# Performance work log

Measured on AMD Instinct MI355X. Metric: run time of the kernel, lower is better.

The kernel has to match this reference:

```python
import jax, jax.numpy as jnp
from jax import lax
import numpy as np

MAX_ITER = 5          # init: max_iter
KSIZE = 3             # init: kernel_size
WEIGHT = 1.0          # init: weight_components
K_COMP = 64           # max number of tracked components (bars) per (b, c)


def setup_inputs() -> dict:
    key = jax.random.key(0)
    k1, k2 = jax.random.split(key)
    predictions = jax.random.normal(k1, (4, 4, 512, 512), dtype=jnp.float32)
    targets = jax.random.randint(k2, (4, 512, 512), 0, 4, dtype=jnp.int32)
    return {"predictions": predictions, "targets": targets}


def _box_sum(x):
    # all-ones KSIZE x KSIZE depthwise conv with SAME zero padding == windowed sum
    return lax.reduce_window(x, 0.0, lax.add, (1, 1, KSIZE, KSIZE), (1, 1, 1, 1), 'SAME')


def _erode(x):
    return (_box_sum(x) == float(KSIZE * KSIZE)).astype(x.dtype)


def _dilate(x):
    return (_box_sum(x) > 0).astype(x.dtype)


def _label_components(fg):
    # fg: bool [B, C, H, W]. 4-connected CCL via min-label propagation to fixpoint;
    # each component gets label = min linear index of its pixels, background = H*W.
    B, C, H, W = fg.shape
    sentinel = jnp.int32(H * W)
    idx = jnp.arange(H * W, dtype=jnp.int32).reshape(1, 1, H, W)
    init = jnp.where(fg, idx, sentinel)

    def nmin(l):
        up = jnp.pad(l, ((0, 0), (0, 0), (1, 0), (0, 0)), constant_values=H * W)[:, :, :-1, :]
        dn = jnp.pad(l, ((0, 0), (0, 0), (0, 1), (0, 0)), constant_values=H * W)[:, :, 1:, :]
        lf = jnp.pad(l, ((0, 0), (0, 0), (0, 0), (1, 0)), constant_values=H * W)[:, :, :, :-1]
        rt = jnp.pad(l, ((0, 0), (0, 0), (0, 0), (0, 1)), constant_values=H * W)[:, :, :, 1:]
        return jnp.minimum(jnp.minimum(up, dn), jnp.minimum(lf, rt))

    def cond(carry):
        return carry[1]

    def body(carry):
        l, _ = carry
        new = jnp.where(fg, jnp.minimum(l, nmin(l)), sentinel)
        return new, jnp.any(new != l)

    labels, _ = lax.while_loop(cond, body, (init, jnp.array(True)))
    return labels


def _component_sizes(im):
    # im: float 0/1 [B, C, H, W] -> top-K_COMP component sizes (sorted desc) [B, C, K_COMP]
    B, C, H, W = im.shape
    HW = H * W
    fg = im > 0.5
    labels = _label_components(fg)
    lab = labels.reshape(B * C, HW)
    w = fg.astype(jnp.float32).reshape(B * C, HW)
    seg = jax.vmap(lambda l, ww: jax.ops.segment_sum(ww, l, num_segments=HW + 1))(lab, w)
    sizes = seg[:, :HW]                      # drop background bucket (label == HW)
    top = lax.top_k(sizes, K_COMP)[0]        # sorted component sizes (barcode at this filtration step)
    return top.reshape(B, C, K_COMP)


def _barcodes(bm):
    # bm: [B, C, H, W] binary maps. Build erosion/dilation filtration exactly as the
    # torch module: image at index max_iter//2 is the original, indices above are
    # successive erosions, indices below are successive dilations.
    mid = MAX_ITER // 2
    imgs = [None] * MAX_ITER
    imgs[mid] = bm
    cur = bm
    for t in range(mid):
        cur = _erode(cur)
        imgs[mid + t + 1] = cur
    cur = bm
    for t in range(mid):
        cur = _dilate(cur)
        imgs[mid - t - 1] = cur
    return jnp.stack([_component_sizes(im) for im in imgs], axis=0)  # [T, B, C, K]


def reference(predictions, targets):
    B, C, H, W = predictions.shape
    prob = jax.nn.softmax(predictions, axis=1)
    pred_cls = jnp.argmax(prob, axis=1)                       # [B, H, W]
    cls = jnp.arange(C, dtype=pred_cls.dtype).reshape(1, -1, 1, 1)
    bp = (pred_cls[:, None] == cls).astype(jnp.float32)       # [B, C, H, W]
    bt = (targets[:, None] == cls).astype(jnp.float32)
    bar_p = _barcodes(bp)                                     # [T, B, C, K]
    bar_t = _barcodes(bt)
    # barcode (persistence-diagram) L1 distance, components matched by size rank,
    # weighted by weight_components; reduction='none' -> per-sample loss [B]
    losses = WEIGHT * jnp.sum(jnp.abs(bar_p - bar_t), axis=(0, 2, 3))
    return losses
```

## Files before the change

kernel.cpp:

```cpp
#include <hip/hip_runtime.h>
#include <stdint.h>

typedef unsigned long long u64;

#define BB   4
#define CC   4
#define HHH  512
#define WWW  512
#define HW   (HHH*WWW)
#define NIMG (BB*CC)
#define NSRC 2
#define NLVL 5
#define NB   (NLVL*NIMG)
#define KTOP 64
#define NBIN 4096
#define WPI  4096
#define SLICE ((size_t)NSRC*NIMG*WPI)
#define TROWS 32
#define TPX  (TROWS*WWW)
#define TWORDS (TROWS*8)
#define NTILE 16
#define NSEAM (NTILE-1)
#define RCAP 8192
#define NGTAG (1 << 30)


__device__ __forceinline__ void unite(int* L, int a, int b) {
  bool done = false;
  do {
    { int p = L[a]; while (p != a) { int gp = L[p]; L[a] = gp; a = gp; p = L[a]; } }
    { int p = L[b]; while (p != b) { int gp = L[p]; L[b] = gp; b = gp; p = L[b]; } }
    if (a < b) {
      int old = atomicMin(&L[b], a);
      done = (old == b);
      b = old;
    } else if (b < a) {
      int old = atomicMin(&L[a], b);
      done = (old == a);
      a = old;
    } else {
      done = true;
    }
  } while (!done);
}

__device__ __forceinline__ int runstart_bit(u64 w, int k) {
  u64 lowz = ~w & ((k == 0) ? 0ull : ((1ull << k) - 1));
  return lowz ? (64 - __clzll(lowz)) : 0;
}

__device__ __forceinline__ u64 morph_word(u64 c0, u64 cm, u64 cp, u64 u0, u64 um, u64 up_,
                                          u64 d0, u64 dm, u64 dp, int erode) {
  u64 v, vm, vp;
  if (erode) {
    v = u0 & c0 & d0; vm = um & cm & dm; vp = up_ & cp & dp;
    return v & ((v << 1) | (vm >> 63)) & ((v >> 1) | (vp << 63));
  } else {
    v = u0 | c0 | d0; vm = um | cm | dm; vp = up_ | cp | dp;
    return v | (v << 1) | (vm >> 63) | (v >> 1) | (vp << 63);
  }
}


__global__ void k_base_mask_bits(const float* __restrict__ pred, const int* __restrict__ tgt,
                                 u64* __restrict__ bm) {
  int i = blockIdx.x * blockDim.x + threadIdx.x;
  if (i >= BB * HW) return;
  int b  = i >> 18;
  int hw = i & (HW - 1);
  float p0 = pred[(b * CC + 0) * HW + hw];
  float p1 = pred[(b * CC + 1) * HW + hw];
  float p2 = pred[(b * CC + 2) * HW + hw];
  float p3 = pred[(b * CC + 3) * HW + hw];
  int amax = 0; float best = p0;
  if (p1 > best) { best = p1; amax = 1; }
  if (p2 > best) { best = p2; amax = 2; }
  if (p3 > best) { best = p3; amax = 3; }
  int tg = tgt[i];
  int lane = threadIdx.x & 63;
  u64* bp = bm + (size_t)(2 * NSRC + 0) * NIMG * WPI;
  u64* bt = bm + (size_t)(2 * NSRC + 1) * NIMG * WPI;
#pragma unroll
  for (int c = 0; c < CC; ++c) {
    u64 wp = __ballot(amax == c);
    u64 wt = __ballot(tg == c);
    if (lane == 0) {
      int wi = ((b * CC + c) << 12) + (hw >> 6);
      bp[wi] = wp;
      bt[wi] = wt;
    }
  }
}

__global__ void k_morph2(u64* __restrict__ bm) {
  __shared__ u64 a[68 * 8];
  __shared__ u64 bsh[66 * 8];
  int blk = blockIdx.x;
  int erode = (blk < 256);
  int blk2 = blk & 255;
  int band = blk2 & 7;
  int imgi = blk2 >> 3;
  int r0 = band * 64;
  const u64* ip = bm + 2 * SLICE + ((size_t)imgi << 12);
  u64* o1 = bm + (erode ? 3 : 1) * SLICE + ((size_t)imgi << 12);
  u64* o2 = bm + (erode ? 4 : 0) * SLICE + ((size_t)imgi << 12);
  int t = threadIdx.x;
  for (int k = t; k < 68 * 8; k += 256) {
    int rr = r0 - 2 + (k >> 3);
    a[k] = (rr >= 0 && rr < HHH) ? ip[rr * 8 + (k & 7)] : 0;
  }
  __syncthreads();
  for (int k = t; k < 66 * 8; k += 256) {
    int j = k >> 3, wc = k & 7;
    int rr = r0 - 1 + j;
    if (rr < 0 || rr >= HHH) { bsh[k] = 0; continue; }
    int ai = (j + 1) * 8 + wc;
    bsh[k] = morph_word(a[ai], wc ? a[ai - 1] : 0, (wc < 7) ? a[ai + 1] : 0,
                        a[ai - 8], wc ? a[ai - 9] : 0, (wc < 7) ? a[ai - 7] : 0,
                        a[ai + 8], wc ? a[ai + 7] : 0, (wc < 7) ? a[ai + 9] : 0, erode);
  }
  __syncthreads();
  for (int k = t; k < 512; k += 256) {
    int j = k >> 3, wc = k & 7;
    int bi = (j + 1) * 8 + wc;
    o1[(r0 + j) * 8 + wc] = bsh[bi];
    o2[(r0 + j) * 8 + wc] =
        morph_word(bsh[bi], wc ? bsh[bi - 1] : 0, (wc < 7) ? bsh[bi + 1] : 0,
                   bsh[bi - 8], wc ? bsh[bi - 9] : 0, (wc < 7) ? bsh[bi - 7] : 0,
                   bsh[bi + 8], wc ? bsh[bi + 7] : 0, (wc < 7) ? bsh[bi + 9] : 0, erode);
  }
}


__global__ __launch_bounds__(1024) void k_ccl_tile(const u64* __restrict__ bm, int src,
                                                   int* __restrict__ labels,
                                                   int* __restrict__ counts,
                                                   int* __restrict__ rootbuf,
                                                   int* __restrict__ rootcnt) {
  __shared__ int par[TPX];
  __shared__ u64 w[TWORDS];
  __shared__ int anyfg, rc;
  int t = threadIdx.x;
  int tile = blockIdx.x;
  int lvl = tile >> 8;
  int img = (tile >> 4) & 15;
  int tin = tile & 15;
  int bimg = tile >> 4;
  int trow0 = tin * TROWS;
  const u64* ib = bm + ((size_t)((lvl * NSRC + src) * NIMG + img) << 12);
  if (t == 0) { anyfg = 0; rc = 0; }
  __syncthreads();
  if (t < TWORDS) {
    u64 wd = ib[trow0 * 8 + t];
    w[t] = wd;
    if (wd) {
      anyfg = 1;
      int segbase = ((t >> 3) << 9) + ((t & 7) << 6);
      u64 hm = wd & ~(wd << 1);
      while (hm) {
        int k = __ffsll(hm) - 1; hm &= hm - 1;
        par[segbase + k] = segbase + k;
      }
    }
  }
  __syncthreads();
  if (!anyfg) { if (t == 0) rootcnt[tile] = 0; return; }
  int wave = t >> 6, lane = t & 63;
  for (int i = wave; i < TWORDS; i += 16) {
    u64 r0 = w[i];
    if (!r0) continue;
    int row = i >> 3, wc = i & 7;
    int segbase = (row << 9) + (wc << 6);
    u64 prev = wc ? w[i - 1] : 0;
    if (lane == 0 && (r0 & 1) && (prev >> 63))
      unite(par, segbase, segbase - 64 + runstart_bit(prev, 63));
    if (row) {
      u64 up = w[i - 8];
      if (up) {
        u64 upprev = wc ? w[i - 9] : 0;
        u64 lsr0 = (r0 << 1) | (prev >> 63);
        u64 lsup = (up << 1) | (upprev >> 63);
        u64 need = r0 & up & ~(lsr0 & lsup);
        if ((need >> lane) & 1)
          unite(par, segbase + runstart_bit(r0, lane),
                     segbase - 512 + runstart_bit(up, lane));
      }
    }
  }
  __syncthreads();
  int off = trow0 * WWW;
  int* L = labels + (bimg << 18) + off;
  for (int i = wave; i < TWORDS; i += 16) {
    u64 wd = w[i];
    if (!wd) continue;
    u64 hm = wd & ~(wd << 1);
    if ((hm >> lane) & 1) {
      int p = ((i >> 3) << 9) + ((i & 7) << 6) + lane;
      int r = p;
      int q = par[r] & 16383;
      while (q != r) { r = q; q = par[r] & 16383; }
      u64 inv = ~(wd >> lane);
      int len = inv ? (__ffsll(inv) - 1) : (64 - lane);
      atomicAdd(&par[r], len << 14);
      int row = i >> 3;
      if (r == p) {
        int idx = atomicAdd(&rc, 1);
        rootbuf[tile * RCAP + idx] = off + p;
        L[p] = off + p;
      } else if (row == 0 || row == TROWS - 1) {
        L[p] = off + r;
      }
    }
  }
  __syncthreads();
  int rcv = rc;
  int base = bimg << 18;
  for (int e = t; e < rcv; e += 1024) {
    int p = rootbuf[tile * RCAP + e] - off;
    counts[base + off + p] = par[p] >> 14;
  }
  if (t == 0) rootcnt[tile] = rcv;
}


__global__ void k_seam_merge(const u64* __restrict__ bm, int src, int* __restrict__ labels) {
  int gid = blockIdx.x * blockDim.x + threadIdx.x;
  int sw = gid >> 6;
  if (sw >= NLVL * NIMG * NSEAM * 8) return;
  int lane = threadIdx.x & 63;
  int lvl = sw / (NIMG * NSEAM * 8);
  int rem = sw - lvl * (NIMG * NSEAM * 8);
  int img = rem / (NSEAM * 8);
  int rem2 = rem - img * (NSEAM * 8);
  int seam = rem2 >> 3, wc = rem2 & 7;
  int rowb = (seam + 1) * TROWS;
  const u64* ib = bm + ((size_t)((lvl * NSRC + src) * NIMG + img) << 12);
  int wb = rowb * 8 + wc;
  u64 r0 = ib[wb];
  if (!r0) return;
  u64 up = ib[wb - 8];
  if (!up) return;
  u64 prev = wc ? ib[wb - 1] : 0;
  u64 upprev = wc ? ib[wb - 9] : 0;
  u64 lsr0 = (r0 << 1) | (prev >> 63);
  u64 lsup = (up << 1) | (upprev >> 63);
  u64 need = r0 & up & ~(lsr0 & lsup);
  if ((need >> lane) & 1) {
    int* L = labels + ((lvl * NIMG + img) << 18);
    int segbase = (rowb << 9) + (wc << 6);
    unite(L, segbase + runstart_bit(r0, lane), segbase - 512 + runstart_bit(up, lane));
  }
}


__global__ __launch_bounds__(256) void k_fixup(const int* __restrict__ rootcnt,
                                               int* __restrict__ rootbuf,
                                               const int* __restrict__ labels,
                                               int* __restrict__ counts,
                                               int* __restrict__ hist,
                                               int* __restrict__ lcount) {
  int tile = blockIdx.x;
  int bimg = tile >> 4;
  int tin = tile & 15;
  int t = threadIdx.x;
  hist[bimg * NBIN + tin * 256 + t] = 0;
  if (t == 0 && tin == 0) lcount[bimg] = 0;
  int n = rootcnt[tile];
  const int* L = labels + (bimg << 18);
  int* cnt = counts + (bimg << 18);
  for (int e = t; e < n; e += 256) {
    int r = rootbuf[tile * RCAP + e];
    int g = r;
    int q = L[g];
    while (q != g) { g = q; q = L[g]; }
    if (g != r) {
      atomicAdd(&cnt[g], cnt[r]);
      rootbuf[tile * RCAP + e] = r | NGTAG;
    }
  }
}


__global__ __launch_bounds__(256) void k_tile_hist(const int* __restrict__ rootcnt,
                                                   const int* __restrict__ rootbuf,
                                                   const int* __restrict__ counts,
                                                   int* __restrict__ hist,
                                                   int* __restrict__ lcount,
                                                   int* __restrict__ lsizes) {
  __shared__ int lh[NBIN];
  int t = threadIdx.x;
  for (int k = t; k < NBIN; k += 256) lh[k] = 0;
  __syncthreads();
  int tile = blockIdx.x;
  int bimg = tile >> 4;
  int n = rootcnt[tile];
  const int* cnt = counts + (bimg << 18);
  for (int e = t; e < n; e += 256) {
    int r = rootbuf[tile * RCAP + e];
    if (r & NGTAG) continue;
    int s = cnt[r];
    if (s <= NBIN) atomicAdd(&lh[s - 1], 1);
    else {
      int idx = atomicAdd(&lcount[bimg], 1);
      if (idx < KTOP) lsizes[bimg * KTOP + idx] = s;
    }
  }
  __syncthreads();
  int* gh = hist + bimg * NBIN;
  for (int k = t; k < NBIN; k += 256)
    if (lh[k]) atomicAdd(&gh[k], lh[k]);
}


__global__ __launch_bounds__(1024) void k_top64(const int* __restrict__ hist,
                                                const int* __restrict__ lcount,
                                                const int* __restrict__ lsizes,
                                                float* __restrict__ top, int src) {
  __shared__ int lh[NBIN];
  __shared__ int sc[1024];
  __shared__ int ls[KTOP];
  int bimg = blockIdx.x;
  int t = threadIdx.x;
  const int* gh = hist + bimg * NBIN;
  for (int k = t; k < NBIN; k += 1024) lh[k] = gh[k];
  int n = lcount[bimg];
  if (n > KTOP) n = KTOP;
  if (t < KTOP) ls[t] = (t < n) ? lsizes[bimg * KTOP + t] : 0;
  int lvl = bimg >> 4, im = bimg & 15;
  float* tp = top + ((size_t)(src * NLVL + lvl) * NIMG + im) * KTOP;
  if (t < KTOP) tp[t] = 0.f;
  __syncthreads();
  if (t < n) {
    int myv = ls[t], rank = 0;
    for (int j = 0; j < n; ++j) {
      int vj = ls[j];
      rank += (vj > myv) || (vj == myv && j < t);
    }
    tp[rank] = (float)myv;
  }
  int base = NBIN - 4 * (t + 1);
  int c = lh[base] + lh[base + 1] + lh[base + 2] + lh[base + 3];
  sc[t] = c;
  __syncthreads();
  for (int off = 1; off < 1024; off <<= 1) {
    int v = (t >= off) ? sc[t - off] : 0;
    __syncthreads();
    sc[t] += v;
    __syncthreads();
  }
  int pos = n + sc[t] - c;
  if (pos < KTOP && c > 0) {
    for (int k = 3; k >= 0 && pos < KTOP; --k) {
      int s = base + k + 1;
      int hc = lh[base + k];
      while (hc-- > 0 && pos < KTOP) tp[pos++] = (float)s;
    }
  }
}

__global__ void k_loss(const float* __restrict__ top, float* __restrict__ out) {
  int b = blockIdx.x;
  int t = threadIdx.x;
  float acc = 0.f;
  const int TOT = NLVL * CC * KTOP;
  for (int e = t; e < TOT; e += 256) {
    int k = e & (KTOP - 1);
    int rest = e >> 6;
    int c = rest & (CC - 1);
    int lvl = rest >> 2;
    int img = b * CC + c;
    size_t iP = ((size_t)(0 * NLVL + lvl) * NIMG + img) * KTOP + k;
    size_t iT = ((size_t)(1 * NLVL + lvl) * NIMG + img) * KTOP + k;
    acc += fabsf(top[iP] - top[iT]);
  }
  __shared__ float r[256];
  r[t] = acc;
  __syncthreads();
  for (int off = 128; off > 0; off >>= 1) {
    if (t < off) r[t] += r[t + off];
    __syncthreads();
  }
  if (t == 0) out[b] = r[0];
}


extern "C" void kernel_launch(void* const* d_in, const int* in_sizes, int n_in,
                              void* d_out, int out_size, void* d_ws, size_t ws_size,
                              hipStream_t stream) {
  const float* pred = (const float*)d_in[0];
  const int*   tgt  = (const int*)d_in[1];
  float* out = (float*)d_out;

  uint8_t* ws = (uint8_t*)d_ws;
  size_t off = 0;
  u64* bmAll   = (u64*)(ws + off); off += (size_t)NLVL * NSRC * NIMG * WPI * 8;
  int* labels  = (int*)(ws + off); off += (size_t)NB * HW * 4;
  int* counts  = (int*)(ws + off); off += (size_t)NB * HW * 4;
  int* rootbuf = (int*)(ws + off); off += (size_t)NB * NTILE * RCAP * 4;
  int* rootcnt = (int*)(ws + off); off += (size_t)NB * NTILE * 4;
  int* hist    = (int*)(ws + off); off += (size_t)NB * NBIN * 4;
  int* lcount  = (int*)(ws + off); off += (size_t)NB * 4;
  int* lsizes  = (int*)(ws + off); off += (size_t)NB * KTOP * 4;
  float* top   = (float*)(ws + off); off += (size_t)NSRC * NLVL * NIMG * KTOP * 4;

  k_base_mask_bits<<<(BB * HW) / 256, 256, 0, stream>>>(pred, tgt, bmAll);
  k_morph2<<<512, 256, 0, stream>>>(bmAll);

  for (int src = 0; src < NSRC; ++src) {
    k_ccl_tile  <<<NB * NTILE, 1024, 0, stream>>>(bmAll, src, labels, counts, rootbuf, rootcnt);
    k_seam_merge<<<(NLVL * NIMG * NSEAM * 8 * 64) / 256, 256, 0, stream>>>(bmAll, src, labels);
    k_fixup     <<<NB * NTILE, 256, 0, stream>>>(rootcnt, rootbuf, labels, counts, hist, lcount);
    k_tile_hist <<<NB * NTILE, 256, 0, stream>>>(rootcnt, rootbuf, counts, hist, lcount, lsizes);
    k_top64     <<<NB, 1024, 0, stream>>>(hist, lcount, lsizes, top, src);
  }

  k_loss<<<BB, 256, 0, stream>>>(top, out);
}
```

Baseline: 195.3 us.

## Use compact per-tile root IDs for global union-find and merge both sources per launch

Tile CCL roots now get compact slot IDs through a shared-memory bitmap plus a prefix-sum, replacing pixel-indexed labels and counts arrays. Global union-find runs over a small per-image root array, and tile boundary rows record root slots so seam merging can look them up. Both sources (prediction and target) are processed in single launches instead of a host loop, which halves the launch count and gives each launch more blocks. Tile blocks are ordered so the middle level is scheduled first. The cost is extra prefix-scan and sync work inside the tile kernel.

```diff
diff --git a/kernel.cpp b/kernel.cpp
--- a/kernel.cpp
+++ b/kernel.cpp
@@ -2,6 +2,7 @@
 #include <stdint.h>
 
 typedef unsigned long long u64;
+typedef unsigned int u32;
 
 #define BB   4
 #define CC   4
@@ -12,6 +13,7 @@
 #define NSRC 2
 #define NLVL 5
 #define NB   (NLVL*NIMG)
+#define NSIMG (NSRC*NB)
 #define KTOP 64
 #define NBIN 4096
 #define WPI  4096
@@ -22,7 +24,7 @@
 #define NTILE 16
 #define NSEAM (NTILE-1)
 #define RCAP 8192
-#define NGTAG (1 << 30)
+#define GSP  (NTILE*RCAP)
 
 
 __device__ __forceinline__ void unite(int* L, int a, int b) {
@@ -47,6 +49,10 @@
 __device__ __forceinline__ int runstart_bit(u64 w, int k) {
   u64 lowz = ~w & ((k == 0) ? 0ull : ((1ull << k) - 1));
   return lowz ? (64 - __clzll(lowz)) : 0;
+}
+
+__device__ __forceinline__ int lvl_of_slot(int s) {
+  return s == 0 ? 2 : s == 1 ? 0 : s == 2 ? 1 : s == 3 ? 3 : 4;
 }
 
 __device__ __forceinline__ u64 morph_word(u64 c0, u64 cm, u64 cp, u64 u0, u64 um, u64 up_,
@@ -78,8 +84,8 @@
   if (p3 > best) { best = p3; amax = 3; }
   int tg = tgt[i];
   int lane = threadIdx.x & 63;
-  u64* bp = bm + (size_t)(2 * NSRC + 0) * NIMG * WPI;
-  u64* bt = bm + (size_t)(2 * NSRC + 1) * NIMG * WPI;
+  u64* bp = bm + 2 * SLICE;
+  u64* bt = bm + 2 * SLICE + (size_t)NIMG * WPI;
 #pragma unroll
   for (int c = 0; c < CC; ++c) {
     u64 wp = __ballot(amax == c);
@@ -132,30 +138,36 @@
 }
 
 
-__global__ __launch_bounds__(1024) void k_ccl_tile(const u64* __restrict__ bm, int src,
-                                                   int* __restrict__ labels,
-                                                   int* __restrict__ counts,
-                                                   int* __restrict__ rootbuf,
+__global__ __launch_bounds__(1024) void k_ccl_tile(const u64* __restrict__ bm,
+                                                   int* __restrict__ bound,
+                                                   int* __restrict__ gparent,
+                                                   int* __restrict__ sizes,
                                                    int* __restrict__ rootcnt) {
   __shared__ int par[TPX];
   __shared__ u64 w[TWORDS];
-  __shared__ int anyfg, rc;
-  int t = threadIdx.x;
-  int tile = blockIdx.x;
-  int lvl = tile >> 8;
-  int img = (tile >> 4) & 15;
-  int tin = tile & 15;
-  int bimg = tile >> 4;
+  __shared__ u32 rb32[TWORDS * 2];
+  __shared__ int rcnt[256];
+  __shared__ int anyfg;
+  int t = threadIdx.x;
+  int idx = blockIdx.x;
+  int lvl = lvl_of_slot(idx >> 9);
+  int rem = idx & 511;
+  int src = rem >> 8;
+  int img = (rem >> 4) & 15;
+  int tin = rem & 15;
+  int simg = src * NB + lvl * NIMG + img;
+  int tile = simg * NTILE + tin;
   int trow0 = tin * TROWS;
   const u64* ib = bm + ((size_t)((lvl * NSRC + src) * NIMG + img) << 12);
-  if (t == 0) { anyfg = 0; rc = 0; }
+  if (t == 0) anyfg = 0;
+  if (t < 512) rb32[t] = 0;
   __syncthreads();
   if (t < TWORDS) {
     u64 wd = ib[trow0 * 8 + t];
     w[t] = wd;
     if (wd) {
       anyfg = 1;
-      int segbase = ((t >> 3) << 9) + ((t & 7) << 6);
+      int segbase = t << 6;
       u64 hm = wd & ~(wd << 1);
       while (hm) {
         int k = __ffsll(hm) - 1; hm &= hm - 1;
@@ -170,7 +182,7 @@
     u64 r0 = w[i];
     if (!r0) continue;
     int row = i >> 3, wc = i & 7;
-    int segbase = (row << 9) + (wc << 6);
+    int segbase = i << 6;
     u64 prev = wc ? w[i - 1] : 0;
     if (lane == 0 && (r0 & 1) && (prev >> 63))
       unite(par, segbase, segbase - 64 + runstart_bit(prev, 63));
@@ -188,51 +200,78 @@
     }
   }
   __syncthreads();
-  int off = trow0 * WWW;
-  int* L = labels + (bimg << 18) + off;
   for (int i = wave; i < TWORDS; i += 16) {
     u64 wd = w[i];
     if (!wd) continue;
     u64 hm = wd & ~(wd << 1);
     if ((hm >> lane) & 1) {
-      int p = ((i >> 3) << 9) + ((i & 7) << 6) + lane;
+      int p = (i << 6) + lane;
       int r = p;
       int q = par[r] & 16383;
       while (q != r) { r = q; q = par[r] & 16383; }
       u64 inv = ~(wd >> lane);
       int len = inv ? (__ffsll(inv) - 1) : (64 - lane);
       atomicAdd(&par[r], len << 14);
-      int row = i >> 3;
-      if (r == p) {
-        int idx = atomicAdd(&rc, 1);
-        rootbuf[tile * RCAP + idx] = off + p;
-        L[p] = off + p;
-      } else if (row == 0 || row == TROWS - 1) {
-        L[p] = off + r;
+      if (r == p) atomicOr(&rb32[p >> 5], 1u << (p & 31));
+    }
+  }
+  __syncthreads();
+  if (t < 256) rcnt[t] = __popcll(((u64)rb32[2 * t + 1] << 32) | rb32[2 * t]);
+  __syncthreads();
+  for (int off2 = 1; off2 < 256; off2 <<= 1) {
+    int v = 0;
+    if (t < 256 && t >= off2) v = rcnt[t - off2];
+    __syncthreads();
+    if (t < 256) rcnt[t] += v;
+    __syncthreads();
+  }
+  if (wave < 16) {
+    int ii = wave;
+    int i = (ii < 8) ? ii : (240 + ii);
+    u64 wd = w[i];
+    if (wd) {
+      u64 hm = wd & ~(wd << 1);
+      if ((hm >> lane) & 1) {
+        int p = (i << 6) + lane;
+        int r = p;
+        int q = par[r] & 16383;
+        while (q != r) { r = q; q = par[r] & 16383; }
+        int wi = r >> 6;
+        u64 rbw = ((u64)rb32[2 * wi + 1] << 32) | rb32[2 * wi];
+        int slot = rcnt[wi] - __popcll(rbw) +
+                   __popcll(rbw & (((u64)1 << (r & 63)) - 1));
+        bound[(size_t)tile * 1024 + (ii < 8 ? 0 : 512) + ((i & 7) << 6) + lane] =
+            tin * RCAP + slot;
       }
     }
   }
-  __syncthreads();
-  int rcv = rc;
-  int base = bimg << 18;
-  for (int e = t; e < rcv; e += 1024) {
-    int p = rootbuf[tile * RCAP + e] - off;
-    counts[base + off + p] = par[p] >> 14;
-  }
-  if (t == 0) rootcnt[tile] = rcv;
-}
-
-
-__global__ void k_seam_merge(const u64* __restrict__ bm, int src, int* __restrict__ labels) {
-  int gid = blockIdx.x * blockDim.x + threadIdx.x;
-  int sw = gid >> 6;
-  if (sw >= NLVL * NIMG * NSEAM * 8) return;
+  int gbase = simg * GSP;
+  for (int i = wave; i < TWORDS; i += 16) {
+    u64 rbw = ((u64)rb32[2 * i + 1] << 32) | rb32[2 * i];
+    if (!((rbw >> lane) & 1)) continue;
+    int p = (i << 6) + lane;
+    int slot = rcnt[i] - __popcll(rbw) + __popcll(rbw & (((u64)1 << lane) - 1));
+    int gid = tin * RCAP + slot;
+    sizes[gbase + gid] = par[p] >> 14;
+    gparent[gbase + gid] = gid;
+  }
+  if (t == 0) rootcnt[tile] = rcnt[255];
+}
+
+
+__global__ void k_seam_merge(const u64* __restrict__ bm, const int* __restrict__ bound,
+                             int* __restrict__ gparent) {
+  int gid_t = blockIdx.x * blockDim.x + threadIdx.x;
+  int sw = gid_t >> 6;
+  if (sw >= NSRC * NLVL * NIMG * NSEAM * 8) return;
   int lane = threadIdx.x & 63;
-  int lvl = sw / (NIMG * NSEAM * 8);
-  int rem = sw - lvl * (NIMG * NSEAM * 8);
-  int img = rem / (NSEAM * 8);
-  int rem2 = rem - img * (NSEAM * 8);
-  int seam = rem2 >> 3, wc = rem2 & 7;
+  int src = sw / (NLVL * NIMG * NSEAM * 8);
+  int rem = sw % (NLVL * NIMG * NSEAM * 8);
+  int lvl = rem / (NIMG * NSEAM * 8);
+  int rem2 = rem % (NIMG * NSEAM * 8);
+  int img = rem2 / (NSEAM * 8);
+  int rem3 = rem2 % (NSEAM * 8);
+  int seam = rem3 >> 3, wc = rem3 & 7;
   int rowb = (seam + 1) * TROWS;
   const u64* ib = bm + ((size_t)((lvl * NSRC + src) * NIMG + img) << 12);
   int wb = rowb * 8 + wc;
@@ -246,44 +285,43 @@
   u64 lsup = (up << 1) | (upprev >> 63);
   u64 need = r0 & up & ~(lsr0 & lsup);
   if ((need >> lane) & 1) {
-    int* L = labels + ((lvl * NIMG + img) << 18);
-    int segbase = (rowb << 9) + (wc << 6);
-    unite(L, segbase + runstart_bit(r0, lane), segbase - 512 + runstart_bit(up, lane));
+    int simg = src * NB + lvl * NIMG + img;
+    const int* bnd = bound + (size_t)simg * NTILE * 1024;
+    int col_a = (wc << 6) + runstart_bit(r0, lane);
+    int col_b = (wc << 6) + runstart_bit(up, lane);
+    int ga = bnd[(seam + 1) * 1024 + col_a];
+    int gb = bnd[seam * 1024 + 512 + col_b];
+    unite(gparent + (size_t)simg * GSP, ga, gb);
   }
 }
 
 
 __global__ __launch_bounds__(256) void k_fixup(const int* __restrict__ rootcnt,
-                                               int* __restrict__ rootbuf,
-                                               const int* __restrict__ labels,
-                                               int* __restrict__ counts,
+                                               int* __restrict__ gparent,
+                                               int* __restrict__ sizes,
                                                int* __restrict__ hist,
                                                int* __restrict__ lcount) {
   int tile = blockIdx.x;
-  int bimg = tile >> 4;
-  int tin = tile & 15;
-  int t = threadIdx.x;
-  hist[bimg * NBIN + tin * 256 + t] = 0;
-  if (t == 0 && tin == 0) lcount[bimg] = 0;
+  int simg = tile >> 4, tin = tile & 15;
+  int t = threadIdx.x;
+  hist[simg * NBIN + tin * 256 + t] = 0;
+  if (t == 0 && tin == 0) lcount[simg] = 0;
   int n = rootcnt[tile];
-  const int* L = labels + (bimg << 18);
-  int* cnt = counts + (bimg << 18);
+  int* G = gparent + (size_t)simg * GSP;
+  int* S = sizes + (size_t)simg * GSP;
   for (int e = t; e < n; e += 256) {
-    int r = rootbuf[tile * RCAP + e];
-    int g = r;
-    int q = L[g];
-    while (q != g) { g = q; q = L[g]; }
-    if (g != r) {
-      atomicAdd(&cnt[g], cnt[r]);
-      rootbuf[tile * RCAP + e] = r | NGTAG;
-    }
+    int gid = tin * RCAP + e;
+    int g = gid;
+    int q = G[g];
+    while (q != g) { g = q; q = G[g]; }
+    if (g != gid) atomicAdd(&S[g], S[gid]);
   }
 }
 
 
 __global__ __launch_bounds__(256) void k_tile_hist(const int* __restrict__ rootcnt,
-                                                   const int* __restrict__ rootbuf,
-                                                   const int* __restrict__ counts,
+                                                   const int* __restrict__ gparent,
+                                                   const int* __restrict__ sizes,
                                                    int* __restrict__ hist,
                                                    int* __restrict__ lcount,
                                                    int* __restrict__ lsizes) {
@@ -292,21 +330,23 @@
   for (int k = t; k < NBIN; k += 256) lh[k] = 0;
   __syncthreads();
   int tile = blockIdx.x;
-  int bimg = tile >> 4;
+  int simg = tile >> 4, tin = tile & 15;
   int n = rootcnt[tile];
-  const int* cnt = counts + (bimg << 18);
+  const int* G = gparent + (size_t)simg * GSP;
+  const int* S = sizes + (size_t)simg * GSP;
   for (int e = t; e < n; e += 256) {
-    int r = rootbuf[tile * RCAP + e];
-    if (r & NGTAG) continue;
-    int s = cnt[r];
-    if (s <= NBIN) atomicAdd(&lh[s - 1], 1);
-    else {
-      int idx = atomicAdd(&lcount[bimg], 1);
-      if (idx < KTOP) lsizes[bimg * KTOP + idx] = s;
-    }
-  }
-  __syncthreads();
-  int* gh = hist + bimg * NBIN;
+    int gid = tin * RCAP + e;
+    if (G[gid] == gid) {
+      int s = S[gid];
+      if (s <= NBIN) atomicAdd(&lh[s - 1], 1);
+      else {
+        int idxl = atomicAdd(&lcount[simg], 1);
+        if (idxl < KTOP) lsizes[simg * KTOP + idxl] = s;
+      }
+    }
+  }
+  __syncthreads();
+  int* gh = hist + simg * NBIN;
   for (int k = t; k < NBIN; k += 256)
     if (lh[k]) atomicAdd(&gh[k], lh[k]);
 }
@@ -315,18 +355,20 @@
 __global__ __launch_bounds__(1024) void k_top64(const int* __restrict__ hist,
                                                 const int* __restrict__ lcount,
                                                 const int* __restrict__ lsizes,
-                                                float* __restrict__ top, int src) {
+                                                float* __restrict__ top) {
   __shared__ int lh[NBIN];
   __shared__ int sc[1024];
   __shared__ int ls[KTOP];
-  int bimg = blockIdx.x;
-  int t = threadIdx.x;
-  const int* gh = hist + bimg * NBIN;
+  int simg = blockIdx.x;
+  int t = threadIdx.x;
+  const int* gh = hist + simg * NBIN;
   for (int k = t; k < NBIN; k += 1024) lh[k] = gh[k];
-  int n = lcount[bimg];
+  int n = lcount[simg];
   if (n > KTOP) n = KTOP;
-  if (t < KTOP) ls[t] = (t < n) ? lsizes[bimg * KTOP + t] : 0;
-  int lvl = bimg >> 4, im = bimg & 15;
+  if (t < KTOP) ls[t] = (t < n) ? lsizes[simg * KTOP + t] : 0;
+  int src = simg / NB;
+  int w2 = simg % NB;
+  int lvl = w2 >> 4, im = w2 & 15;
   float* tp = top + ((size_t)(src * NLVL + lvl) * NIMG + im) * KTOP;
   if (t < KTOP) tp[t] = 0.f;
   __syncthreads();
@@ -393,26 +435,24 @@
 
   uint8_t* ws = (uint8_t*)d_ws;
   size_t off = 0;
-  u64* bmAll   = (u64*)(ws + off); off += (size_t)NLVL * NSRC * NIMG * WPI * 8;
-  int* labels  = (int*)(ws + off); off += (size_t)NB * HW * 4;
-  int* counts  = (int*)(ws + off); off += (size_t)NB * HW * 4;
-  int* rootbuf = (int*)(ws + off); off += (size_t)NB * NTILE * RCAP * 4;
-  int* rootcnt = (int*)(ws + off); off += (size_t)NB * NTILE * 4;
-  int* hist    = (int*)(ws + off); off += (size_t)NB * NBIN * 4;
-  int* lcount  = (int*)(ws + off); off += (size_t)NB * 4;
-  int* lsizes  = (int*)(ws + off); off += (size_t)NB * KTOP * 4;
+  u64* bmAll   = (u64*)(ws + off); off += (size_t)NLVL * SLICE * 8;
+  int* bound   = (int*)(ws + off); off += (size_t)NSIMG * NTILE * 1024 * 4;
+  int* gparent = (int*)(ws + off); off += (size_t)NSIMG * GSP * 4;
+  int* sizes   = (int*)(ws + off); off += (size_t)NSIMG * GSP * 4;
+  int* rootcnt = (int*)(ws + off); off += (size_t)NSIMG * NTILE * 4;
+  int* hist    = (int*)(ws + off); off += (size_t)NSIMG * NBIN * 4;
+  int* lcount  = (int*)(ws + off); off += (size_t)NSIMG * 4;
+  int* lsizes  = (int*)(ws + off); off += (size_t)NSIMG * KTOP * 4;
   float* top   = (float*)(ws + off); off += (size_t)NSRC * NLVL * NIMG * KTOP * 4;
 
   k_base_mask_bits<<<(BB * HW) / 256, 256, 0, stream>>>(pred, tgt, bmAll);
   k_morph2<<<512, 256, 0, stream>>>(bmAll);
 
-  for (int src = 0; src < NSRC; ++src) {
-    k_ccl_tile  <<<NB * NTILE, 1024, 0, stream>>>(bmAll, src, labels, counts, rootbuf, rootcnt);
-    k_seam_merge<<<(NLVL * NIMG * NSEAM * 8 * 64) / 256, 256, 0, stream>>>(bmAll, src, labels);
-    k_fixup     <<<NB * NTILE, 256, 0, stream>>>(rootcnt, rootbuf, labels, counts, hist, lcount);
-    k_tile_hist <<<NB * NTILE, 256, 0, stream>>>(rootcnt, rootbuf, counts, hist, lcount, lsizes);
-    k_top64     <<<NB, 1024, 0, stream>>>(hist, lcount, lsizes, top, src);
-  }
+  k_ccl_tile  <<<NSIMG * NTILE, 1024, 0, stream>>>(bmAll, bound, gparent, sizes, rootcnt);
+  k_seam_merge<<<(NSRC * NLVL * NIMG * NSEAM * 8 * 64) / 256, 256, 0, stream>>>(bmAll, bound, gparent);
+  k_fixup     <<<NSIMG * NTILE, 256, 0, stream>>>(rootcnt, gparent, sizes, hist, lcount);
+  k_tile_hist <<<NSIMG * NTILE, 256, 0, stream>>>(rootcnt, gparent, sizes, hist, lcount, lsizes);
+  k_top64     <<<NSIMG, 1024, 0, stream>>>(hist, lcount, lsizes, top);
 
   k_loss<<<BB, 256, 0, stream>>>(top, out);
 }
```

Measured after the change: 158.6 us. 18.8% less time.
